# Kernel optimization log

Hardware: AMD Instinct MI355X
Metric: run time of the kernel (lower is better)

Reference implementation:

```python
import jax, jax.numpy as jnp
import numpy as np

EPS = 1e-6

def _rms_norm(x, w):
    rms = jnp.sqrt(jnp.mean(x * x, axis=-1, keepdims=True) + EPS)
    return x / rms * w

def _rotate_half(x):
    x1, x2 = jnp.split(x, 2, axis=-1)
    return jnp.concatenate([-x2, x1], axis=-1)

def _apply_rope(qk, cos, sin):
    return qk * cos + _rotate_half(qk) * sin

def setup_inputs() -> dict:
    key = jax.random.key(0)
    ks = jax.random.split(key, 4)
    B, N, C, H = 4, 2048, 1024, 16
    hd = C // H
    x = jax.random.normal(ks[0], (B, N, C), dtype=jnp.float32)
    rope_cos = jax.random.uniform(ks[1], (1, 1, N, hd), dtype=jnp.float32)
    rope_sin = jax.random.uniform(ks[2], (1, 1, N, hd), dtype=jnp.float32)
    w_qkv = jax.random.normal(ks[3], (3 * C, C), dtype=jnp.float32) * (C ** -0.5)
    w_proj = jax.random.normal(jax.random.fold_in(key, 10), (C, C), dtype=jnp.float32) * (C ** -0.5)
    b_proj = jnp.zeros((C,), dtype=jnp.float32)
    q_norm_w = jnp.ones((hd,), dtype=jnp.float32)
    k_norm_w = jnp.ones((hd,), dtype=jnp.float32)
    return {"x": x, "rope_cos": rope_cos, "rope_sin": rope_sin, "w_qkv": w_qkv,
            "w_proj": w_proj, "b_proj": b_proj, "q_norm_w": q_norm_w, "k_norm_w": k_norm_w}

def reference(x, rope_cos, rope_sin, w_qkv, w_proj, b_proj, q_norm_w, k_norm_w):
    B, N, C = x.shape
    H = 16
    hd = C // H
    scale = hd ** -0.5
    qkv = jnp.einsum('bnc,dc->bnd', x, w_qkv)          # [B,N,3C]
    qkv = qkv.reshape(B, N, 3, H, hd).transpose(2, 0, 3, 1, 4)  # [3,B,H,N,hd]
    q, k, v = qkv[0], qkv[1], qkv[2]
    q = _rms_norm(q, q_norm_w)
    k = _rms_norm(k, k_norm_w)
    q = _apply_rope(q, rope_cos, rope_sin)
    k = _apply_rope(k, rope_cos, rope_sin)
    attn = jnp.einsum('bhqd,bhkd->bhqk', q, k) * scale
    attn = jax.nn.softmax(attn, axis=-1)
    out = jnp.einsum('bhqk,bhkd->bhqd', attn, v)        # [B,H,N,hd]
    out = out.transpose(0, 2, 1, 3).reshape(B, N, C)
    return jnp.einsum('bnc,dc->bnd', out, w_proj) + b_proj
```

## Files before the change

### kernel.cpp

```cpp
#include <hip/hip_runtime.h>
#include <stdint.h>
#include <math.h>

typedef unsigned short u16;
typedef __attribute__((ext_vector_type(8))) short short8;
typedef __attribute__((ext_vector_type(4))) float floatx4;
typedef __attribute__((ext_vector_type(4))) unsigned short ushort4v;

#define MFMA16(a, b, c) __builtin_amdgcn_mfma_f32_16x16x32_bf16(a, b, c, 0, 0, 0)

constexpr int B_ = 4, N_ = 2048, C_ = 1024, H_ = 16, HD = 64;
constexpr size_t SZ_X = (size_t)B_ * N_ * C_;
constexpr size_t SZ_WQKV = (size_t)3 * C_ * C_;
constexpr size_t SZ_WPROJ = (size_t)C_ * C_;
constexpr size_t SZ_QKV = (size_t)B_ * H_ * N_ * HD;

#define QSCALE 0.1803368801111204f

__device__ __forceinline__ u16 f2bf(float f) {
  union { float f; uint32_t u; } c; c.f = f;
  uint32_t u = c.u;
  return (u16)((u + 0x7FFFu + ((u >> 16) & 1u)) >> 16);
}
__device__ __forceinline__ u16 f2bf_fast(float f) {
  union { float f; uint32_t u; } c; c.f = f;
  return (u16)((c.u + 0x8000u) >> 16);
}
__device__ __forceinline__ void async16(const u16* g, u16* l) {
  __builtin_amdgcn_global_load_lds(
      (const __attribute__((address_space(1))) void*)g,
      (__attribute__((address_space(3))) void*)l, 16, 0, 0);
}

__global__ __launch_bounds__(256) void cvt_bf16(const float* __restrict__ in,
                                                u16* __restrict__ out, int n4) {
  int i = blockIdx.x * 256 + threadIdx.x;
  if (i >= n4) return;
  float4 v = ((const float4*)in)[i];
  ushort4v o;
  o.x = f2bf(v.x); o.y = f2bf(v.y); o.z = f2bf(v.z); o.w = f2bf(v.w);
  ((ushort4v*)out)[i] = o;
}

template <int MODE>
__global__ __launch_bounds__(256) void gemm_bt(
    const u16* __restrict__ A, const u16* __restrict__ Bm, int K,
    u16* __restrict__ qb, u16* __restrict__ kb, u16* __restrict__ vtb,
    float* __restrict__ outf, const float* __restrict__ bias, int N,
    const float* __restrict__ cosp, const float* __restrict__ sinp,
    const float* __restrict__ qw, const float* __restrict__ kw) {
  const int tid = threadIdx.x;
  const int wave = tid >> 6;
  const int lane = tid & 63;
  const int quad = lane >> 4;
  const int l16 = lane & 15;
  const int bm0 = blockIdx.x * 128;
  const int bn0 = blockIdx.y * 128;
  const int wm = (wave >> 1) * 64;
  const int wn = (wave & 1) * 64;

  __shared__ __align__(16) u16 As[2][128 * 32];
  __shared__ __align__(16) u16 Bs[2][128 * 32];

  floatx4 acc[4][4];
#pragma unroll
  for (int i = 0; i < 4; ++i)
#pragma unroll
    for (int j = 0; j < 4; ++j)
#pragma unroll
      for (int r = 0; r < 4; ++r) acc[i][j][r] = 0.f;

  auto stage = [&](int k0, int buf) {
#pragma unroll
    for (int j = 0; j < 2; ++j) {
      const int seg = tid + j * 256;
      const int row = seg >> 2;
      const int ks = (seg & 3) * 8;
      u16* la = As[buf] + (size_t)(wave * 64 + j * 256) * 8;
      u16* lb = Bs[buf] + (size_t)(wave * 64 + j * 256) * 8;
      async16(A + (size_t)(bm0 + row) * K + k0 + ks, la);
      async16(Bm + (size_t)(bn0 + row) * K + k0 + ks, lb);
    }
  };

  const int niter = K >> 5;
  stage(0, 0);
  for (int kt = 0; kt < niter; ++kt) {
    __syncthreads();
    if (kt + 1 < niter) stage((kt + 1) << 5, (kt + 1) & 1);
    const u16* as = As[kt & 1];
    const u16* bs = Bs[kt & 1];

    short8 af[4], bf[4];
#pragma unroll
    for (int t = 0; t < 4; ++t)
      af[t] = *(const short8*)(as + (wm + t * 16 + l16) * 32 + quad * 8);
#pragma unroll
    for (int t = 0; t < 4; ++t)
      bf[t] = *(const short8*)(bs + (wn + t * 16 + l16) * 32 + quad * 8);
#pragma unroll
    for (int i = 0; i < 4; ++i)
#pragma unroll
      for (int j = 0; j < 4; ++j)
        acc[i][j] = MFMA16(af[i], bf[j], acc[i][j]);
  }

  if (MODE == 0) {
    const int hb = (bn0 + wn) >> 6;
    const int t = hb >> 4;
    const int h = hb & 15;
    if (t < 2) {
      const float* w = (t == 0) ? qw : kw;
      u16* dstb = (t == 0) ? qb : kb;
      float wv[4];
#pragma unroll
      for (int j = 0; j < 4; ++j) wv[j] = w[j * 16 + l16];
#pragma unroll
      for (int i = 0; i < 4; ++i)
#pragma unroll
        for (int r = 0; r < 4; ++r) {
          const int m = bm0 + wm + i * 16 + quad * 4 + r;
          const int b = m >> 11, tok = m & 2047;
          float ss = 0.f;
#pragma unroll
          for (int j = 0; j < 4; ++j) ss += acc[i][j][r] * acc[i][j][r];
          ss += __shfl_xor(ss, 1);
          ss += __shfl_xor(ss, 2);
          ss += __shfl_xor(ss, 4);
          ss += __shfl_xor(ss, 8);
          const float inv = 1.0f / sqrtf(ss * (1.0f / 64.0f) + 1e-6f);
          float xn[4];
#pragma unroll
          for (int j = 0; j < 4; ++j) xn[j] = acc[i][j][r] * inv * wv[j];
          u16* dst = dstb + ((size_t)(b * 16 + h) * 2048 + tok) * 64;
#pragma unroll
          for (int j = 0; j < 4; ++j) {
            const int e = j * 16 + l16;
            const float cs = cosp[tok * 64 + e];
            const float sn = sinp[tok * 64 + e];
            const float rot = (j < 2) ? -xn[j + 2] : xn[j - 2];
            float o = xn[j] * cs + rot * sn;
            if (t == 0) o *= QSCALE;
            dst[e] = f2bf(o);
          }
        }
    } else {
#pragma unroll
      for (int i = 0; i < 4; ++i)
#pragma unroll
        for (int j = 0; j < 4; ++j)
#pragma unroll
          for (int r = 0; r < 4; ++r) {
            const int m = bm0 + wm + i * 16 + quad * 4 + r;
            const int b = m >> 11, tok = m & 2047;
            const int e = j * 16 + l16;
            vtb[((size_t)(b * 16 + h) * 64 + e) * 2048 + tok] =
                f2bf(acc[i][j][r]);
          }
    }
  } else {
#pragma unroll
    for (int i = 0; i < 4; ++i)
#pragma unroll
      for (int j = 0; j < 4; ++j)
#pragma unroll
        for (int r = 0; r < 4; ++r) {
          const int m = bm0 + wm + i * 16 + quad * 4 + r;
          const int n = bn0 + wn + j * 16 + l16;
          outf[(size_t)m * N + n] = acc[i][j][r] + bias[n];
        }
  }
}

__global__ __launch_bounds__(256) void attn_kernel(
    const u16* __restrict__ qb, const u16* __restrict__ kb,
    const u16* __restrict__ vtb, u16* __restrict__ ob) {
  const int tid = threadIdx.x;
  const int wave = tid >> 6, lane = tid & 63;
  const int quad = lane >> 4, l16 = lane & 15;

  const int id = blockIdx.x + blockIdx.y * 16;
  const int bh = (id & 7) + 8 * ((id >> 3) & 7);
  const int q0 = (id >> 6) * 128;

  __shared__ __align__(16) u16 Ksf[2][64 * 64];
  __shared__ __align__(16) u16 Vsf[2][64 * 64];
  __shared__ __align__(16) u16 Ps[4][2][16 * 72];

  const u16* qptr = qb + (size_t)bh * (2048 * 64);
  const u16* kptr = kb + (size_t)bh * (2048 * 64);
  const u16* vptr = vtb + (size_t)bh * (64 * 2048);

  const int s0 = tid, s1 = tid + 256;
  const int ct0 = s0 >> 7, ct1 = s1 >> 7;
  const int hf0 = (s0 >> 6) & 1, hf1 = (s1 >> 6) & 1;
  const u16* kg0 = kptr + (size_t)(ct0 * 16 + l16) * 64 + hf0 * 32 + quad * 8;
  const u16* kg1 = kptr + (size_t)(ct1 * 16 + l16) * 64 + hf1 * 32 + quad * 8;
  const u16* vg0 = vptr + (size_t)(ct0 * 16 + l16) * 2048 + hf0 * 32 + quad * 8;
  const u16* vg1 = vptr + (size_t)(ct1 * 16 + l16) * 2048 + hf1 * 32 + quad * 8;
  const int lo0 = (wave * 64) * 8;
  const int lo1 = (256 + wave * 64) * 8;

  short8 aq[2][2];
#pragma unroll
  for (int sub = 0; sub < 2; ++sub) {
    const int qrow = q0 + wave * 32 + sub * 16 + l16;
#pragma unroll
    for (int hf = 0; hf < 2; ++hf)
      aq[sub][hf] =
          *(const short8*)(qptr + (size_t)qrow * 64 + hf * 32 + quad * 8);
  }

  short8 ones;
#pragma unroll
  for (int j = 0; j < 8; ++j) ones[j] = (short)0x3F80;

  floatx4 o[2][4], ol[2];
#pragma unroll
  for (int sub = 0; sub < 2; ++sub) {
#pragma unroll
    for (int r = 0; r < 4; ++r) ol[sub][r] = 0.f;
#pragma unroll
    for (int et = 0; et < 4; ++et)
#pragma unroll
      for (int r = 0; r < 4; ++r) o[sub][et][r] = 0.f;
  }

  async16(kg0, Ksf[0] + lo0);
  async16(kg1, Ksf[0] + lo1);
  async16(vg0, Vsf[0] + lo0);
  async16(vg1, Vsf[0] + lo1);

  for (int it = 0; it < 32; ++it) {
    __syncthreads();
    if (it + 1 < 32) {
      const int n1 = (it + 1) * 64;
      const int b1 = (it + 1) & 1;
      async16(kg0 + (size_t)n1 * 64, Ksf[b1] + lo0);
      async16(kg1 + (size_t)n1 * 64, Ksf[b1] + lo1);
      async16(vg0 + n1, Vsf[b1] + lo0);
      async16(vg1 + n1, Vsf[b1] + lo1);
    }
    const u16* Kt = Ksf[it & 1];
    const u16* Vt = Vsf[it & 1];

#pragma unroll
    for (int t = 0; t < 4; ++t) {
      const short8 kf0 = *(const short8*)(Kt + t * 1024 + lane * 8);
      const short8 kf1 = *(const short8*)(Kt + t * 1024 + 512 + lane * 8);
#pragma unroll
      for (int sub = 0; sub < 2; ++sub) {
        floatx4 z;
#pragma unroll
        for (int r = 0; r < 4; ++r) z[r] = 0.f;
        z = MFMA16(kf0, aq[sub][0], z);
        z = MFMA16(kf1, aq[sub][1], z);
        ushort4v pk;
        pk.x = f2bf_fast(__builtin_amdgcn_exp2f(z[0]));
        pk.y = f2bf_fast(__builtin_amdgcn_exp2f(z[1]));
        pk.z = f2bf_fast(__builtin_amdgcn_exp2f(z[2]));
        pk.w = f2bf_fast(__builtin_amdgcn_exp2f(z[3]));
        *(ushort4v*)(Ps[wave][sub] + l16 * 72 + t * 16 + quad * 4) = pk;
      }
    }

    __asm__ volatile("s_waitcnt lgkmcnt(0)" ::: "memory");

    short8 pa[2][2];
#pragma unroll
    for (int sub = 0; sub < 2; ++sub) {
      pa[sub][0] = *(const short8*)(Ps[wave][sub] + l16 * 72 + quad * 8);
      pa[sub][1] = *(const short8*)(Ps[wave][sub] + l16 * 72 + 32 + quad * 8);
    }

#pragma unroll
    for (int et = 0; et < 4; ++et) {
      const short8 vb0 = *(const short8*)(Vt + et * 1024 + lane * 8);
      const short8 vb1 = *(const short8*)(Vt + et * 1024 + 512 + lane * 8);
#pragma unroll
      for (int sub = 0; sub < 2; ++sub) {
        o[sub][et] = MFMA16(pa[sub][0], vb0, o[sub][et]);
        o[sub][et] = MFMA16(pa[sub][1], vb1, o[sub][et]);
      }
    }
#pragma unroll
    for (int sub = 0; sub < 2; ++sub) {
      ol[sub] = MFMA16(pa[sub][0], ones, ol[sub]);
      ol[sub] = MFMA16(pa[sub][1], ones, ol[sub]);
    }
  }

  const int b = bh >> 4, h = bh & 15;
#pragma unroll
  for (int sub = 0; sub < 2; ++sub) {
    float inv[4];
#pragma unroll
    for (int r = 0; r < 4; ++r) inv[r] = 1.0f / ol[sub][r];
#pragma unroll
    for (int et = 0; et < 4; ++et)
#pragma unroll
      for (int r = 0; r < 4; ++r) {
        const int row = q0 + wave * 32 + sub * 16 + quad * 4 + r;
        const int e = et * 16 + l16;
        ob[((size_t)b * 2048 + row) * 1024 + h * 64 + e] =
            f2bf(o[sub][et][r] * inv[r]);
      }
  }
}

extern "C" void kernel_launch(void* const* d_in, const int* in_sizes, int n_in,
                              void* d_out, int out_size, void* d_ws, size_t ws_size,
                              hipStream_t stream) {
  const float* x     = (const float*)d_in[0];
  const float* cosp  = (const float*)d_in[1];
  const float* sinp  = (const float*)d_in[2];
  const float* wqkv  = (const float*)d_in[3];
  const float* wproj = (const float*)d_in[4];
  const float* bias  = (const float*)d_in[5];
  const float* qw    = (const float*)d_in[6];
  const float* kw    = (const float*)d_in[7];
  float* out = (float*)d_out;

  u16* xb     = (u16*)d_ws;
  u16* wqkvb  = xb + SZ_X;
  u16* wprojb = wqkvb + SZ_WQKV;
  u16* qb     = wprojb + SZ_WPROJ;
  u16* kb     = qb + SZ_QKV;
  u16* vtb    = kb + SZ_QKV;
  u16* ob     = vtb + SZ_QKV;

  cvt_bf16<<<(int)(SZ_X / 4 / 256), 256, 0, stream>>>(x, xb, (int)(SZ_X / 4));
  cvt_bf16<<<(int)(SZ_WQKV / 4 / 256), 256, 0, stream>>>(wqkv, wqkvb, (int)(SZ_WQKV / 4));
  cvt_bf16<<<(int)(SZ_WPROJ / 4 / 256), 256, 0, stream>>>(wproj, wprojb, (int)(SZ_WPROJ / 4));

  gemm_bt<0><<<dim3(64, 24), 256, 0, stream>>>(xb, wqkvb, 1024, qb, kb, vtb,
                                               nullptr, nullptr, 3072,
                                               cosp, sinp, qw, kw);
  attn_kernel<<<dim3(16, 64), 256, 0, stream>>>(qb, kb, vtb, ob);
  gemm_bt<1><<<dim3(64, 8), 256, 0, stream>>>(ob, wprojb, 1024, nullptr, nullptr,
                                              nullptr, out, bias, 1024,
                                              nullptr, nullptr, nullptr, nullptr);
}
```

Baseline: 312.1 us.

## Double attention query tile per block and replace exp2 with bit-trick bf16 exponent

Each wave in the attention kernel now handles 64 query rows (four 16-row subtiles) instead of 32. K and V fragments are loaded from LDS once per iteration and reused across all subtiles, and the grid is halved with an XCD-aware block-to-head mapping. Each per-subtile P tile is written, read back and consumed by the PV MFMAs immediately, reusing two P buffers. The exp2 plus bf16 rounding is replaced by a single FMA and int conversion that builds bf16 bits of 2^s directly (Schraudolph-style), which is less accurate and fails for very negative scores. The larger tile also raises register pressure and leaves fewer blocks in flight.

```diff
diff --git a/kernel.cpp b/kernel.cpp
--- a/kernel.cpp
+++ b/kernel.cpp
@@ -22,9 +22,8 @@
   uint32_t u = c.u;
   return (u16)((u + 0x7FFFu + ((u >> 16) & 1u)) >> 16);
 }
-__device__ __forceinline__ u16 f2bf_fast(float f) {
-  union { float f; uint32_t u; } c; c.f = f;
-  return (u16)((c.u + 0x8000u) >> 16);
+__device__ __forceinline__ uint32_t p2b(float s) {
+  return (uint32_t)(int)__builtin_fmaf(s, 128.0f, 16250.91f);
 }
 __device__ __forceinline__ void async16(const u16* g, u16* l) {
   __builtin_amdgcn_global_load_lds(
@@ -179,9 +178,11 @@
   const int wave = tid >> 6, lane = tid & 63;
   const int quad = lane >> 4, l16 = lane & 15;
 
-  const int id = blockIdx.x + blockIdx.y * 16;
-  const int bh = (id & 7) + 8 * ((id >> 3) & 7);
-  const int q0 = (id >> 6) * 128;
+  const int id = blockIdx.x + blockIdx.y * 8;
+  const int xcd = id & 7;
+  const int grp = id >> 3;
+  const int bh = xcd * 8 + (grp & 7);
+  const int q0 = (grp >> 3) * 256;
 
   __shared__ __align__(16) u16 Ksf[2][64 * 64];
   __shared__ __align__(16) u16 Vsf[2][64 * 64];
@@ -201,10 +202,10 @@
   const int lo0 = (wave * 64) * 8;
   const int lo1 = (256 + wave * 64) * 8;
 
-  short8 aq[2][2];
-#pragma unroll
-  for (int sub = 0; sub < 2; ++sub) {
-    const int qrow = q0 + wave * 32 + sub * 16 + l16;
+  short8 aq[4][2];
+#pragma unroll
+  for (int sub = 0; sub < 4; ++sub) {
+    const int qrow = q0 + wave * 64 + sub * 16 + l16;
 #pragma unroll
     for (int hf = 0; hf < 2; ++hf)
       aq[sub][hf] =
@@ -215,9 +216,9 @@
 #pragma unroll
   for (int j = 0; j < 8; ++j) ones[j] = (short)0x3F80;
 
-  floatx4 o[2][4], ol[2];
-#pragma unroll
-  for (int sub = 0; sub < 2; ++sub) {
+  floatx4 o[4][4], ol[4];
+#pragma unroll
+  for (int sub = 0; sub < 4; ++sub) {
 #pragma unroll
     for (int r = 0; r < 4; ++r) ol[sub][r] = 0.f;
 #pragma unroll
@@ -244,55 +245,49 @@
     const u16* Kt = Ksf[it & 1];
     const u16* Vt = Vsf[it & 1];
 
+    short8 kf[4][2], vf[4][2];
 #pragma unroll
     for (int t = 0; t < 4; ++t) {
-      const short8 kf0 = *(const short8*)(Kt + t * 1024 + lane * 8);
-      const short8 kf1 = *(const short8*)(Kt + t * 1024 + 512 + lane * 8);
-#pragma unroll
-      for (int sub = 0; sub < 2; ++sub) {
+      kf[t][0] = *(const short8*)(Kt + t * 1024 + lane * 8);
+      kf[t][1] = *(const short8*)(Kt + t * 1024 + 512 + lane * 8);
+    }
+#pragma unroll
+    for (int et = 0; et < 4; ++et) {
+      vf[et][0] = *(const short8*)(Vt + et * 1024 + lane * 8);
+      vf[et][1] = *(const short8*)(Vt + et * 1024 + 512 + lane * 8);
+    }
+
+#pragma unroll
+    for (int sub = 0; sub < 4; ++sub) {
+      u16* pb = Ps[wave][sub & 1];
+#pragma unroll
+      for (int t = 0; t < 4; ++t) {
         floatx4 z;
 #pragma unroll
         for (int r = 0; r < 4; ++r) z[r] = 0.f;
-        z = MFMA16(kf0, aq[sub][0], z);
-        z = MFMA16(kf1, aq[sub][1], z);
-        ushort4v pk;
-        pk.x = f2bf_fast(__builtin_amdgcn_exp2f(z[0]));
-        pk.y = f2bf_fast(__builtin_amdgcn_exp2f(z[1]));
-        pk.z = f2bf_fast(__builtin_amdgcn_exp2f(z[2]));
-        pk.w = f2bf_fast(__builtin_amdgcn_exp2f(z[3]));
-        *(ushort4v*)(Ps[wave][sub] + l16 * 72 + t * 16 + quad * 4) = pk;
+        z = MFMA16(kf[t][0], aq[sub][0], z);
+        z = MFMA16(kf[t][1], aq[sub][1], z);
+        uint2 w;
+        w.x = p2b(z[0]) | (p2b(z[1]) << 16);
+        w.y = p2b(z[2]) | (p2b(z[3]) << 16);
+        *(uint2*)(pb + l16 * 72 + t * 16 + quad * 4) = w;
       }
-    }
-
-    __asm__ volatile("s_waitcnt lgkmcnt(0)" ::: "memory");
-
-    short8 pa[2][2];
-#pragma unroll
-    for (int sub = 0; sub < 2; ++sub) {
-      pa[sub][0] = *(const short8*)(Ps[wave][sub] + l16 * 72 + quad * 8);
-      pa[sub][1] = *(const short8*)(Ps[wave][sub] + l16 * 72 + 32 + quad * 8);
-    }
-
-#pragma unroll
-    for (int et = 0; et < 4; ++et) {
-      const short8 vb0 = *(const short8*)(Vt + et * 1024 + lane * 8);
-      const short8 vb1 = *(const short8*)(Vt + et * 1024 + 512 + lane * 8);
-#pragma unroll
-      for (int sub = 0; sub < 2; ++sub) {
-        o[sub][et] = MFMA16(pa[sub][0], vb0, o[sub][et]);
-        o[sub][et] = MFMA16(pa[sub][1], vb1, o[sub][et]);
+      __asm__ volatile("s_waitcnt lgkmcnt(0)" ::: "memory");
+      const short8 pa0 = *(const short8*)(pb + l16 * 72 + quad * 8);
+      const short8 pa1 = *(const short8*)(pb + l16 * 72 + 32 + quad * 8);
+#pragma unroll
+      for (int et = 0; et < 4; ++et) {
+        o[sub][et] = MFMA16(pa0, vf[et][0], o[sub][et]);
+        o[sub][et] = MFMA16(pa1, vf[et][1], o[sub][et]);
       }
-    }
-#pragma unroll
-    for (int sub = 0; sub < 2; ++sub) {
-      ol[sub] = MFMA16(pa[sub][0], ones, ol[sub]);
-      ol[sub] = MFMA16(pa[sub][1], ones, ol[sub]);
+      ol[sub] = MFMA16(pa0, ones, ol[sub]);
+      ol[sub] = MFMA16(pa1, ones, ol[sub]);
     }
   }
 
   const int b = bh >> 4, h = bh & 15;
 #pragma unroll
-  for (int sub = 0; sub < 2; ++sub) {
+  for (int sub = 0; sub < 4; ++sub) {
     float inv[4];
 #pragma unroll
     for (int r = 0; r < 4; ++r) inv[r] = 1.0f / ol[sub][r];
@@ -300,7 +295,7 @@
     for (int et = 0; et < 4; ++et)
 #pragma unroll
       for (int r = 0; r < 4; ++r) {
-        const int row = q0 + wave * 32 + sub * 16 + quad * 4 + r;
+        const int row = q0 + wave * 64 + sub * 16 + quad * 4 + r;
         const int e = et * 16 + l16;
         ob[((size_t)b * 2048 + row) * 1024 + h * 64 + e] =
             f2bf(o[sub][et][r] * inv[r]);
@@ -336,7 +331,7 @@
   gemm_bt<0><<<dim3(64, 24), 256, 0, stream>>>(xb, wqkvb, 1024, qb, kb, vtb,
                                                nullptr, nullptr, 3072,
                                                cosp, sinp, qw, kw);
-  attn_kernel<<<dim3(16, 64), 256, 0, stream>>>(qb, kb, vtb, ob);
+  attn_kernel<<<dim3(8, 64), 256, 0, stream>>>(qb, kb, vtb, ob);
   gemm_bt<1><<<dim3(64, 8), 256, 0, stream>>>(ob, wprojb, 1024, nullptr, nullptr,
                                               nullptr, out, bias, 1024,
                                               nullptr, nullptr, nullptr, nullptr);
```

New measurement: 332.8 us. 1.07x slower.
